# Optimization experiments

Hardware: AMD Instinct MI355X
Metric: run time of the kernel (lower is better)

The kernel has to match this reference:

```python
import jax, jax.numpy as jnp
import numpy as np

C, K, D_LLM = 32, 16, 768
B, L, D_MODEL = 8, 512, 256
H, D_KEYS = 8, 32
TEMP = 1.0 / np.sqrt(D_KEYS)


def setup_inputs() -> dict:
    key = jax.random.key(0)
    ks = jax.random.split(key, 8)
    topk = jax.random.normal(ks[0], (C, K, D_LLM), dtype=jnp.float32)
    ts_emb = jax.random.normal(ks[1], (B, L, D_MODEL), dtype=jnp.float32)
    probs = jax.random.uniform(ks[2], (B, L, C), dtype=jnp.float32)
    probs = probs / jnp.sum(probs, axis=-1, keepdims=True)  # soft cluster probabilities
    scale = 0.02  # keep pre-softmax logits in a stable range
    q_proj = jax.random.normal(ks[3], (C, H * D_KEYS, D_MODEL + 1), dtype=jnp.float32) * scale
    k_proj = jax.random.normal(ks[4], (C, H * D_KEYS, D_LLM + 1), dtype=jnp.float32) * scale
    v_proj = jax.random.normal(ks[5], (C, H * D_KEYS, D_LLM + 1), dtype=jnp.float32) * scale
    out_w = jax.random.normal(ks[6], (C, H, D_KEYS, D_LLM), dtype=jnp.float32) * scale
    out_b = jax.random.normal(ks[7], (C, D_LLM), dtype=jnp.float32) * scale
    return {"topk_token_embeddings": topk, "ts_emb": ts_emb, "cluster_probs": probs,
            "q_proj": q_proj, "k_proj": k_proj, "v_proj": v_proj,
            "out_w": out_w, "out_b": out_b}


def reference(topk_token_embeddings, ts_emb, cluster_probs, q_proj, k_proj, v_proj, out_w, out_b):
    b, l, _ = ts_emb.shape
    c, k, d_llm = topk_token_embeddings.shape
    # per-cluster Q/K/V projections (weights have an extra trailing bias column)
    q = jnp.einsum('bld,cgd->blcg', ts_emb, q_proj[..., :-1]) + q_proj[..., -1]
    q = q.reshape(b, l, c, H, D_KEYS)
    kk = jnp.einsum('ckd,cgd->kcg', topk_token_embeddings, k_proj[..., :-1]) + k_proj[..., -1]
    kk = kk.reshape(k, c, H, D_KEYS)
    v = jnp.einsum('ckd,cgd->kcg', topk_token_embeddings, v_proj[..., :-1]) + v_proj[..., -1]
    v = v.reshape(k, c, H, D_KEYS)
    # cross attention over the k retrieved tokens, per cluster and head
    att = jnp.einsum('blchd,kchd->bchlk', q, kk)  # (B,c,H,L,k)
    att = jax.nn.softmax(TEMP * att, axis=-1)  # dropout disabled (eval)
    out_v = jnp.einsum('bchlk,kchd->bclhd', att, v)
    aligned = jnp.einsum('bclhd,chde->blce', out_v, out_w) + out_b  # (B,L,c,d_llm)
    fused = jnp.sum(aligned * cluster_probs[:, :, :, None], axis=-2)  # (B,L,d_llm)
    return fused
```

## Files before the change

kernel.cpp:

```cpp
#include <hip/hip_runtime.h>
#include <hip/hip_bf16.h>

#define C_   32
#define K_   16
#define DLLM 768
#define DM   256
#define H_   8
#define DK   32
#define G_   256
#define BL   4096
#define NN   4096
#define E_   768
#define LDP  4160
#define TEMPF 0.17677669529663687f
#define SCL2  0.2550348647f

typedef __attribute__((ext_vector_type(8))) short bf16x8;
typedef __attribute__((ext_vector_type(4))) float f32x4;
typedef unsigned int u32;

__device__ __forceinline__ unsigned short f2bf(float f) {
    unsigned int u = __float_as_uint(f);
    unsigned int r = (u + 0x7fffu + ((u >> 16) & 1u)) >> 16;
    return (unsigned short)r;
}
__device__ __forceinline__ float bf2f(unsigned int u) {
    return __uint_as_float(u << 16);
}

__device__ __forceinline__ void gl16(const void* g, void* l) {
    __builtin_amdgcn_global_load_lds(
        (const __attribute__((address_space(1))) u32*)g,
        (__attribute__((address_space(3))) u32*)l, 16, 0, 0);
}

__global__ __launch_bounds__(256) void k1_kv(const float* __restrict__ topk,
                                             const float* __restrict__ kp,
                                             const float* __restrict__ vp,
                                             float* __restrict__ kk,
                                             float* __restrict__ vv) {
    const int cl  = blockIdx.x;
    const int nq  = blockIdx.y;
    const int mat = blockIdx.z;
    const float* src = mat ? vp : kp;
    float* dst       = mat ? vv : kk;

    const int t = threadIdx.x;
    const int lane = t & 63, w = t >> 6;
    const int c15 = lane & 15, gg = lane >> 4;

    __shared__ unsigned short a_lds[16 * 776];
#pragma unroll
    for (int i = 0; i < 12; ++i) {
        const int e = (i * 256 + t) * 4;
        const int r = e / 768, d = e - r * 768;
        float4 v4 = *reinterpret_cast<const float4*>(topk + (size_t)cl * 12288 + e);
        unsigned u0, u1;
        asm("v_cvt_pk_bf16_f32 %0, %1, %2" : "=v"(u0) : "v"(v4.x), "v"(v4.y));
        asm("v_cvt_pk_bf16_f32 %0, %1, %2" : "=v"(u1) : "v"(v4.z), "v"(v4.w));
        uint2 p; p.x = u0; p.y = u1;
        *reinterpret_cast<uint2*>(&a_lds[r * 776 + d]) = p;
    }
    __syncthreads();

    const int gcol = nq * 64 + w * 16 + c15;
    const float* bp = src + (size_t)(cl * G_ + gcol) * (DLLM + 1);
    const float bias = bp[DLLM];

    f32x4 acc = {};
    float4 b0 = *reinterpret_cast<const float4*>(bp + gg * 8);
    float4 b1 = *reinterpret_cast<const float4*>(bp + gg * 8 + 4);
#pragma unroll
    for (int s = 0; s < 24; ++s) {
        float4 n0, n1;
        if (s < 23) {
            n0 = *reinterpret_cast<const float4*>(bp + (s + 1) * 32 + gg * 8);
            n1 = *reinterpret_cast<const float4*>(bp + (s + 1) * 32 + gg * 8 + 4);
        }
        union { unsigned u[4]; bf16x8 v; } bb;
        asm("v_cvt_pk_bf16_f32 %0, %1, %2" : "=v"(bb.u[0]) : "v"(b0.x), "v"(b0.y));
        asm("v_cvt_pk_bf16_f32 %0, %1, %2" : "=v"(bb.u[1]) : "v"(b0.z), "v"(b0.w));
        asm("v_cvt_pk_bf16_f32 %0, %1, %2" : "=v"(bb.u[2]) : "v"(b1.x), "v"(b1.y));
        asm("v_cvt_pk_bf16_f32 %0, %1, %2" : "=v"(bb.u[3]) : "v"(b1.z), "v"(b1.w));
        bf16x8 af = *reinterpret_cast<const bf16x8*>(&a_lds[c15 * 776 + s * 32 + gg * 8]);
        acc = __builtin_amdgcn_mfma_f32_16x16x32_bf16(af, bb.v, acc, 0, 0, 0);
        b0 = n0; b1 = n1;
    }

#pragma unroll
    for (int i = 0; i < 4; ++i) {
        const int row = gg * 4 + i;
        dst[(size_t)(cl * K_ + row) * G_ + gcol] = acc[i] + bias;
    }
}

__global__ __launch_bounds__(256) void k0_cvt(const float* __restrict__ ts,
                                              const float* __restrict__ probs,
                                              const float* __restrict__ outb,
                                              unsigned short* __restrict__ tsb,
                                              unsigned short* __restrict__ P,
                                              unsigned short* __restrict__ VWt) {
    const int bid = blockIdx.x, t = threadIdx.x;
    if (bid < 1024) {
        const int idx = bid * 1024 + t * 4;
        float4 v = *reinterpret_cast<const float4*>(ts + idx);
        uint2 o;
        o.x = f2bf(v.x) | ((unsigned)f2bf(v.y) << 16);
        o.y = f2bf(v.z) | ((unsigned)f2bf(v.w) << 16);
        *reinterpret_cast<uint2*>(tsb + idx) = o;
    } else if (bid < 1056) {
        const int b2 = bid - 1024;
        const int row = b2 * 128 + (t >> 1);
        const int ch = (t & 1) * 16;
        unsigned short o[16];
#pragma unroll
        for (int j = 0; j < 16; ++j) o[j] = f2bf(probs[row * 32 + ch + j]);
        uint4 u0, u1;
        u0.x = o[0] | (o[1] << 16);  u0.y = o[2] | (o[3] << 16);
        u0.z = o[4] | (o[5] << 16);  u0.w = o[6] | (o[7] << 16);
        u1.x = o[8] | (o[9] << 16);  u1.y = o[10] | (o[11] << 16);
        u1.z = o[12] | (o[13] << 16); u1.w = o[14] | (o[15] << 16);
        unsigned short* dst = P + (size_t)row * LDP + 4096 + ch;
        *reinterpret_cast<uint4*>(dst) = u0;
        *reinterpret_cast<uint4*>(dst + 8) = u1;
        uint4 z = {0u, 0u, 0u, 0u};
        unsigned short* pz = P + (size_t)row * LDP + 4128 + ch;
        *reinterpret_cast<uint4*>(pz) = z;
        *reinterpret_cast<uint4*>(pz + 8) = z;
    } else {
        const int idx = (bid - 1056) * 256 + t;
        const int e = idx >> 5, cc = idx & 31;
        VWt[(size_t)e * LDP + 4096 + cc] = f2bf(outb[cc * E_ + e]);
        VWt[(size_t)e * LDP + 4128 + cc] = 0;
    }
}

__global__ __launch_bounds__(768) void k23(const float* __restrict__ qp,
                                           const float* __restrict__ kk,
                                           const float* __restrict__ ow,
                                           const float* __restrict__ vv,
                                           unsigned short* __restrict__ A2t,
                                           float* __restrict__ abias,
                                           unsigned short* __restrict__ VWt) {
    const int c = blockIdx.x, h = blockIdx.y;
    const int t = threadIdx.x;
    __shared__ float kk_l[K_][DK];
    __shared__ float v_l[K_][DK];
    __shared__ float bq_l[DK];
    if (t < 512) {
        int k = t / DK, d = t % DK;
        kk_l[k][d] = kk[(size_t)(c * K_ + k) * G_ + h * DK + d];
        v_l[k][d]  = vv[(size_t)(c * K_ + k) * G_ + h * DK + d];
    }
    if (t < DK)
        bq_l[t] = qp[(size_t)(c * G_ + h * DK + t) * (DM + 1) + DM];
    __syncthreads();
    const int ch = c * H_ + h;
    {
        const int e = t;
        float acc[K_];
#pragma unroll
        for (int k = 0; k < K_; ++k) acc[k] = 0.f;
        for (int d = 0; d < DK; ++d) {
            float w = ow[((size_t)ch * DK + d) * E_ + e];
#pragma unroll
            for (int k = 0; k < K_; ++k) acc[k] += w * v_l[k][d];
        }
#pragma unroll
        for (int k = 0; k < K_; ++k)
            VWt[(size_t)e * LDP + ch * 16 + k] = f2bf(acc[k]);
    }
    if (t < 256) {
        const int m = t;
        float acc[K_];
#pragma unroll
        for (int k = 0; k < K_; ++k) acc[k] = 0.f;
        for (int d = 0; d < DK; ++d) {
            float wq = qp[(size_t)(c * G_ + h * DK + d) * (DM + 1) + m];
#pragma unroll
            for (int k = 0; k < K_; ++k) acc[k] += wq * kk_l[k][d];
        }
#pragma unroll
        for (int k = 0; k < K_; ++k)
            A2t[(size_t)(ch * 16 + k) * DM + m] = f2bf(acc[k] * SCL2);
        if (m < K_) {
            float s = 0.f;
#pragma unroll
            for (int d = 0; d < DK; ++d) s += bq_l[d] * kk_l[m][d];
            abias[ch * 16 + m] = s * SCL2;
        }
    }
}

__global__ __launch_bounds__(256, 2) void k4_att(const unsigned short* __restrict__ A2t,
                                                 const unsigned short* __restrict__ tsb,
                                                 const float* __restrict__ abias,
                                                 const float* __restrict__ probs,
                                                 unsigned short* __restrict__ P) {
    const int n0  = blockIdx.x * 128;
    const int bl0 = blockIdx.y * 256;
    const int t = threadIdx.x;
    const int lane = t & 63, w = t >> 6;
    const int wr = w >> 1, wc = w & 1;
    const int c = lane & 15, g = lane >> 4;
    const int rsl = (c >> 1) & 3;

    __shared__ unsigned short a_l[3][128 * 32];
    __shared__ unsigned short b_l[3][256 * 32];
    __shared__ float ab_l[128];
    __shared__ float pb_l[256];

    if (t < 128) ab_l[t] = abias[n0 + t];
    pb_l[t] = probs[(size_t)(bl0 + t) * C_ + (n0 >> 7)];

    const int srow = t >> 2;
    const int sw = ((t & 3) ^ ((t >> 3) & 3)) * 8;

#define K4_STAGE(buf, kt)                                                         \
    {                                                                             \
        const int col_ = (kt) * 32 + sw;                                          \
        _Pragma("unroll")                                                         \
        for (int j = 0; j < 2; ++j)                                               \
            gl16(A2t + (size_t)(n0 + j * 64 + srow) * DM + col_,                  \
                 &a_l[buf][j * 2048 + t * 8]);                                    \
        _Pragma("unroll")                                                         \
        for (int j = 0; j < 4; ++j)                                               \
            gl16(tsb + (size_t)(bl0 + j * 64 + srow) * DM + col_,                 \
                 &b_l[buf][j * 2048 + t * 8]);                                    \
    }

    K4_STAGE(0, 0)
    K4_STAGE(1, 1)
    asm volatile("s_waitcnt lgkmcnt(0)" ::: "memory");

    f32x4 acc[4][8] = {};

#pragma unroll
    for (int kt = 0; kt < 8; ++kt) {
        const int bcur = kt % 3;
        if (kt < 6) {
            K4_STAGE((kt + 2) % 3, kt + 2)
            asm volatile("s_waitcnt vmcnt(12)" ::: "memory");
        } else if (kt == 6) {
            asm volatile("s_waitcnt vmcnt(6)" ::: "memory");
        } else {
            asm volatile("s_waitcnt vmcnt(0)" ::: "memory");
        }
        asm volatile("s_barrier" ::: "memory");
        bf16x8 af[4], bfr[8];
#pragma unroll
        for (int a = 0; a < 4; ++a)
            af[a] = *reinterpret_cast<const bf16x8*>(
                &a_l[bcur][(wr * 64 + a * 16 + c) * 32 + (g ^ rsl) * 8]);
#pragma unroll
        for (int b = 0; b < 8; ++b)
            bfr[b] = *reinterpret_cast<const bf16x8*>(
                &b_l[bcur][(wc * 128 + b * 16 + c) * 32 + (g ^ rsl) * 8]);
#pragma unroll
        for (int a = 0; a < 4; ++a)
#pragma unroll
            for (int b = 0; b < 8; ++b)
                acc[a][b] = __builtin_amdgcn_mfma_f32_16x16x32_bf16(af[a], bfr[b], acc[a][b], 0, 0, 0);
        if (kt < 7)
            asm volatile("s_barrier" ::: "memory");
    }
#undef K4_STAGE

#pragma unroll
    for (int a = 0; a < 4; ++a) {
        const int nbase = wr * 64 + a * 16 + g * 4;
#pragma unroll
        for (int b = 0; b < 8; ++b) {
            const int bll = wc * 128 + b * 16 + c;
            float e0 = __builtin_amdgcn_exp2f(acc[a][b][0] + ab_l[nbase + 0]);
            float e1 = __builtin_amdgcn_exp2f(acc[a][b][1] + ab_l[nbase + 1]);
            float e2 = __builtin_amdgcn_exp2f(acc[a][b][2] + ab_l[nbase + 2]);
            float e3 = __builtin_amdgcn_exp2f(acc[a][b][3] + ab_l[nbase + 3]);
            float s = (e0 + e1) + (e2 + e3);
            s += __shfl_xor(s, 16);
            s += __shfl_xor(s, 32);
            const float pv = pb_l[bll] * __builtin_amdgcn_rcpf(s);
            unsigned r0, r1;
            float p0 = e0 * pv, p1 = e1 * pv, p2 = e2 * pv, p3 = e3 * pv;
            asm("v_cvt_pk_bf16_f32 %0, %1, %2" : "=v"(r0) : "v"(p0), "v"(p1));
            asm("v_cvt_pk_bf16_f32 %0, %1, %2" : "=v"(r1) : "v"(p2), "v"(p3));
            uint2 o; o.x = r0; o.y = r1;
            *reinterpret_cast<uint2*>(P + (size_t)(bl0 + bll) * LDP + n0 + nbase) = o;
        }
    }
}

__global__ __launch_bounds__(256, 3) void k5_out(const unsigned short* __restrict__ P,
                                                 const unsigned short* __restrict__ VWt,
                                                 unsigned short* __restrict__ part) {
    const int wg = blockIdx.x;
    const int xcd = wg & 7;
    const int local = wg >> 3;
    const int bl0 = (xcd * 4 + (local & 3)) * 128;
    const int e0  = ((local >> 2) & 3) * 192;
    const int ks  = local >> 4;

    const int t = threadIdx.x;
    const int lane = t & 63, w = t >> 6;
    const int wr = w >> 1, wc = w & 1;
    const int c = lane & 15, g = lane >> 4;
    const int rsl = (c >> 1) & 3;

    __shared__ unsigned short a_l[2][128 * 32];
    __shared__ unsigned short b_l[2][192 * 32];

    const int nstart = ks * 704;
    const int nsteps = (ks == 5) ? 20 : 22;

    const int srow = t >> 2;
    const int sw = ((t & 3) ^ ((t >> 3) & 3)) * 8;

#define K5_STAGE(buf, kt)                                                         \
    {                                                                             \
        const int col_ = nstart + (kt) * 32 + sw;                                 \
        _Pragma("unroll")                                                         \
        for (int j = 0; j < 2; ++j)                                               \
            gl16(P + (size_t)(bl0 + j * 64 + srow) * LDP + col_,                  \
                 &a_l[buf][j * 2048 + t * 8]);                                    \
        _Pragma("unroll")                                                         \
        for (int j = 0; j < 3; ++j)                                               \
            gl16(VWt + (size_t)(e0 + j * 64 + srow) * LDP + col_,                 \
                 &b_l[buf][j * 2048 + t * 8]);                                    \
    }

    K5_STAGE(0, 0)

    f32x4 acc[4][6] = {};
    for (int kt = 0; kt < nsteps; ++kt) {
        const int bcur = kt & 1;
        if (kt + 1 < nsteps) {
            K5_STAGE(bcur ^ 1, kt + 1)
            asm volatile("s_waitcnt vmcnt(5)" ::: "memory");
        } else {
            asm volatile("s_waitcnt vmcnt(0)" ::: "memory");
        }
        asm volatile("s_barrier" ::: "memory");
        bf16x8 af[4], bfr[6];
#pragma unroll
        for (int a = 0; a < 4; ++a)
            af[a] = *reinterpret_cast<const bf16x8*>(
                &a_l[bcur][(wr * 64 + a * 16 + c) * 32 + (g ^ rsl) * 8]);
#pragma unroll
        for (int b = 0; b < 6; ++b)
            bfr[b] = *reinterpret_cast<const bf16x8*>(
                &b_l[bcur][(wc * 96 + b * 16 + c) * 32 + (g ^ rsl) * 8]);
#pragma unroll
        for (int a = 0; a < 4; ++a)
#pragma unroll
            for (int b = 0; b < 6; ++b)
                acc[a][b] = __builtin_amdgcn_mfma_f32_16x16x32_bf16(af[a], bfr[b], acc[a][b], 0, 0, 0);
        if (kt + 1 < nsteps)
            asm volatile("s_barrier" ::: "memory");
    }
#undef K5_STAGE

    unsigned short* pp = part + ((size_t)ks * BL + bl0) * E_ + e0;
#pragma unroll
    for (int a = 0; a < 4; ++a)
#pragma unroll
        for (int b = 0; b < 6; ++b)
#pragma unroll
            for (int i = 0; i < 4; ++i)
                pp[(size_t)(wr * 64 + a * 16 + g * 4 + i) * E_ + wc * 96 + b * 16 + c] =
                    f2bf(acc[a][b][i]);
}

__global__ __launch_bounds__(256) void k6_red(const unsigned short* __restrict__ part,
                                              float* __restrict__ out) {
    const size_t base = ((size_t)blockIdx.x * 256 + threadIdx.x) * 8;
    float s[8] = {};
#pragma unroll
    for (int ks = 0; ks < 6; ++ks) {
        uint4 v = *reinterpret_cast<const uint4*>(part + (size_t)ks * (BL * E_) + base);
        const unsigned u[4] = {v.x, v.y, v.z, v.w};
#pragma unroll
        for (int j = 0; j < 4; ++j) {
            s[2 * j]     += bf2f(u[j] & 0xffffu);
            s[2 * j + 1] += bf2f(u[j] >> 16);
        }
    }
    *reinterpret_cast<float4*>(out + base)     = make_float4(s[0], s[1], s[2], s[3]);
    *reinterpret_cast<float4*>(out + base + 4) = make_float4(s[4], s[5], s[6], s[7]);
}

extern "C" void kernel_launch(void* const* d_in, const int* in_sizes, int n_in,
                              void* d_out, int out_size, void* d_ws, size_t ws_size,
                              hipStream_t stream) {
    const float* topk  = (const float*)d_in[0];
    const float* ts    = (const float*)d_in[1];
    const float* probs = (const float*)d_in[2];
    const float* qp    = (const float*)d_in[3];
    const float* kp    = (const float*)d_in[4];
    const float* vp    = (const float*)d_in[5];
    const float* ow    = (const float*)d_in[6];
    const float* ob    = (const float*)d_in[7];
    float* out = (float*)d_out;

    char* wp = (char*)d_ws;
    float* kk            = (float*)wp;           wp += 524288;
    float* vv            = (float*)wp;           wp += 524288;
    float* ab            = (float*)wp;           wp += 16384;
    unsigned short* tsb  = (unsigned short*)wp;  wp += 2097152;
    unsigned short* A2t  = (unsigned short*)wp;  wp += 2097152;
    unsigned short* VWt  = (unsigned short*)wp;  wp += (size_t)E_ * LDP * 2;
    unsigned short* P    = (unsigned short*)wp;  wp += (size_t)BL * LDP * 2;
    unsigned short* part = (unsigned short*)wp;

    k1_kv <<<dim3(32, 4, 2), 256, 0, stream>>>(topk, kp, vp, kk, vv);
    k0_cvt<<<1152,           256, 0, stream>>>(ts, probs, ob, tsb, P, VWt);
    k23   <<<dim3(32, 8),    768, 0, stream>>>(qp, kk, ow, vv, A2t, ab, VWt);
    k4_att<<<dim3(32, 16),   256, 0, stream>>>(A2t, tsb, ab, probs, P);
    k5_out<<<768,            256, 0, stream>>>(P, VWt, part);
    k6_red<<<1536,           256, 0, stream>>>(part, out);
}
```

Baseline: 99.21 us.

## Merge prep kernels, transpose probs, shrink attention tile for occupancy

Folds the K/V projection kernel and the conversion kernel into one launch, which removes a launch and its serialization gap. It adds a block range that transposes cluster_probs so the attention kernel loads per-cluster probabilities with coalesced reads. The attention-logit kernel moves from a 128x256 tile with triple buffering to a 128x128 tile with double buffering. That halves the accumulators and LDS, allowing 4 blocks per CU, and doubles the grid. The trade-off is less reuse of the A2t tile per block and a shallower prefetch pipeline.

```diff
diff --git a/kernel.cpp b/kernel.cpp
--- a/kernel.cpp
+++ b/kernel.cpp
@@ -34,82 +34,81 @@
         (__attribute__((address_space(3))) u32*)l, 16, 0, 0);
 }
 
-__global__ __launch_bounds__(256) void k1_kv(const float* __restrict__ topk,
-                                             const float* __restrict__ kp,
-                                             const float* __restrict__ vp,
-                                             float* __restrict__ kk,
-                                             float* __restrict__ vv) {
-    const int cl  = blockIdx.x;
-    const int nq  = blockIdx.y;
-    const int mat = blockIdx.z;
-    const float* src = mat ? vp : kp;
-    float* dst       = mat ? vv : kk;
-
-    const int t = threadIdx.x;
-    const int lane = t & 63, w = t >> 6;
-    const int c15 = lane & 15, gg = lane >> 4;
-
+__global__ __launch_bounds__(256) void k01(const float* __restrict__ topk,
+                                           const float* __restrict__ kp,
+                                           const float* __restrict__ vp,
+                                           float* __restrict__ kk,
+                                           float* __restrict__ vv,
+                                           const float* __restrict__ ts,
+                                           const float* __restrict__ probs,
+                                           const float* __restrict__ outb,
+                                           unsigned short* __restrict__ tsb,
+                                           unsigned short* __restrict__ P,
+                                           unsigned short* __restrict__ VWt,
+                                           float* __restrict__ probsT) {
+    const int bid = blockIdx.x, t = threadIdx.x;
     __shared__ unsigned short a_lds[16 * 776];
-#pragma unroll
-    for (int i = 0; i < 12; ++i) {
-        const int e = (i * 256 + t) * 4;
-        const int r = e / 768, d = e - r * 768;
-        float4 v4 = *reinterpret_cast<const float4*>(topk + (size_t)cl * 12288 + e);
-        unsigned u0, u1;
-        asm("v_cvt_pk_bf16_f32 %0, %1, %2" : "=v"(u0) : "v"(v4.x), "v"(v4.y));
-        asm("v_cvt_pk_bf16_f32 %0, %1, %2" : "=v"(u1) : "v"(v4.z), "v"(v4.w));
-        uint2 p; p.x = u0; p.y = u1;
-        *reinterpret_cast<uint2*>(&a_lds[r * 776 + d]) = p;
-    }
-    __syncthreads();
-
-    const int gcol = nq * 64 + w * 16 + c15;
-    const float* bp = src + (size_t)(cl * G_ + gcol) * (DLLM + 1);
-    const float bias = bp[DLLM];
-
-    f32x4 acc = {};
-    float4 b0 = *reinterpret_cast<const float4*>(bp + gg * 8);
-    float4 b1 = *reinterpret_cast<const float4*>(bp + gg * 8 + 4);
-#pragma unroll
-    for (int s = 0; s < 24; ++s) {
-        float4 n0, n1;
-        if (s < 23) {
-            n0 = *reinterpret_cast<const float4*>(bp + (s + 1) * 32 + gg * 8);
-            n1 = *reinterpret_cast<const float4*>(bp + (s + 1) * 32 + gg * 8 + 4);
-        }
-        union { unsigned u[4]; bf16x8 v; } bb;
-        asm("v_cvt_pk_bf16_f32 %0, %1, %2" : "=v"(bb.u[0]) : "v"(b0.x), "v"(b0.y));
-        asm("v_cvt_pk_bf16_f32 %0, %1, %2" : "=v"(bb.u[1]) : "v"(b0.z), "v"(b0.w));
-        asm("v_cvt_pk_bf16_f32 %0, %1, %2" : "=v"(bb.u[2]) : "v"(b1.x), "v"(b1.y));
-        asm("v_cvt_pk_bf16_f32 %0, %1, %2" : "=v"(bb.u[3]) : "v"(b1.z), "v"(b1.w));
-        bf16x8 af = *reinterpret_cast<const bf16x8*>(&a_lds[c15 * 776 + s * 32 + gg * 8]);
-        acc = __builtin_amdgcn_mfma_f32_16x16x32_bf16(af, bb.v, acc, 0, 0, 0);
-        b0 = n0; b1 = n1;
-    }
-
-#pragma unroll
-    for (int i = 0; i < 4; ++i) {
-        const int row = gg * 4 + i;
-        dst[(size_t)(cl * K_ + row) * G_ + gcol] = acc[i] + bias;
-    }
-}
-
-__global__ __launch_bounds__(256) void k0_cvt(const float* __restrict__ ts,
-                                              const float* __restrict__ probs,
-                                              const float* __restrict__ outb,
-                                              unsigned short* __restrict__ tsb,
-                                              unsigned short* __restrict__ P,
-                                              unsigned short* __restrict__ VWt) {
-    const int bid = blockIdx.x, t = threadIdx.x;
-    if (bid < 1024) {
-        const int idx = bid * 1024 + t * 4;
+
+    if (bid < 256) {
+        const int cl  = bid & 31;
+        const int nq  = (bid >> 5) & 3;
+        const int mat = bid >> 7;
+        const float* src = mat ? vp : kp;
+        float* dst       = mat ? vv : kk;
+
+        const int lane = t & 63, w = t >> 6;
+        const int c15 = lane & 15, gg = lane >> 4;
+
+#pragma unroll
+        for (int i = 0; i < 12; ++i) {
+            const int e = (i * 256 + t) * 4;
+            const int r = e / 768, d = e - r * 768;
+            float4 v4 = *reinterpret_cast<const float4*>(topk + (size_t)cl * 12288 + e);
+            unsigned u0, u1;
+            asm("v_cvt_pk_bf16_f32 %0, %1, %2" : "=v"(u0) : "v"(v4.x), "v"(v4.y));
+            asm("v_cvt_pk_bf16_f32 %0, %1, %2" : "=v"(u1) : "v"(v4.z), "v"(v4.w));
+            uint2 p; p.x = u0; p.y = u1;
+            *reinterpret_cast<uint2*>(&a_lds[r * 776 + d]) = p;
+        }
+        __syncthreads();
+
+        const int gcol = nq * 64 + w * 16 + c15;
+        const float* bp = src + (size_t)(cl * G_ + gcol) * (DLLM + 1);
+        const float bias = bp[DLLM];
+
+        f32x4 acc = {};
+        float4 b0 = *reinterpret_cast<const float4*>(bp + gg * 8);
+        float4 b1 = *reinterpret_cast<const float4*>(bp + gg * 8 + 4);
+#pragma unroll
+        for (int s = 0; s < 24; ++s) {
+            float4 n0, n1;
+            if (s < 23) {
+                n0 = *reinterpret_cast<const float4*>(bp + (s + 1) * 32 + gg * 8);
+                n1 = *reinterpret_cast<const float4*>(bp + (s + 1) * 32 + gg * 8 + 4);
+            }
+            union { unsigned u[4]; bf16x8 v; } bb;
+            asm("v_cvt_pk_bf16_f32 %0, %1, %2" : "=v"(bb.u[0]) : "v"(b0.x), "v"(b0.y));
+            asm("v_cvt_pk_bf16_f32 %0, %1, %2" : "=v"(bb.u[1]) : "v"(b0.z), "v"(b0.w));
+            asm("v_cvt_pk_bf16_f32 %0, %1, %2" : "=v"(bb.u[2]) : "v"(b1.x), "v"(b1.y));
+            asm("v_cvt_pk_bf16_f32 %0, %1, %2" : "=v"(bb.u[3]) : "v"(b1.z), "v"(b1.w));
+            bf16x8 af = *reinterpret_cast<const bf16x8*>(&a_lds[c15 * 776 + s * 32 + gg * 8]);
+            acc = __builtin_amdgcn_mfma_f32_16x16x32_bf16(af, bb.v, acc, 0, 0, 0);
+            b0 = n0; b1 = n1;
+        }
+#pragma unroll
+        for (int i = 0; i < 4; ++i) {
+            const int row = gg * 4 + i;
+            dst[(size_t)(cl * K_ + row) * G_ + gcol] = acc[i] + bias;
+        }
+    } else if (bid < 1280) {
+        const int idx = (bid - 256) * 1024 + t * 4;
         float4 v = *reinterpret_cast<const float4*>(ts + idx);
         uint2 o;
         o.x = f2bf(v.x) | ((unsigned)f2bf(v.y) << 16);
         o.y = f2bf(v.z) | ((unsigned)f2bf(v.w) << 16);
         *reinterpret_cast<uint2*>(tsb + idx) = o;
-    } else if (bid < 1056) {
-        const int b2 = bid - 1024;
+    } else if (bid < 1312) {
+        const int b2 = bid - 1280;
         const int row = b2 * 128 + (t >> 1);
         const int ch = (t & 1) * 16;
         unsigned short o[16];
@@ -127,11 +126,27 @@
         unsigned short* pz = P + (size_t)row * LDP + 4128 + ch;
         *reinterpret_cast<uint4*>(pz) = z;
         *reinterpret_cast<uint4*>(pz + 8) = z;
-    } else {
-        const int idx = (bid - 1056) * 256 + t;
+    } else if (bid < 1408) {
+        const int idx = (bid - 1312) * 256 + t;
         const int e = idx >> 5, cc = idx & 31;
         VWt[(size_t)e * LDP + 4096 + cc] = f2bf(outb[cc * E_ + e]);
         VWt[(size_t)e * LDP + 4128 + cc] = 0;
+    } else {
+        float* tl = reinterpret_cast<float*>(a_lds);
+        const int bl0p = (bid - 1408) * 128;
+#pragma unroll
+        for (int i = 0; i < 16; ++i) {
+            const int row = i * 8 + (t >> 5);
+            const int cc = t & 31;
+            tl[row * 33 + cc] = probs[(size_t)(bl0p + row) * C_ + cc];
+        }
+        __syncthreads();
+#pragma unroll
+        for (int j = 0; j < 16; ++j) {
+            const int cc = j * 2 + (t >> 7);
+            const int bl = t & 127;
+            probsT[(size_t)cc * BL + bl0p + bl] = tl[bl * 33 + cc];
+        }
     }
 }
 
@@ -192,26 +207,26 @@
     }
 }
 
-__global__ __launch_bounds__(256, 2) void k4_att(const unsigned short* __restrict__ A2t,
+__global__ __launch_bounds__(256, 4) void k4_att(const unsigned short* __restrict__ A2t,
                                                  const unsigned short* __restrict__ tsb,
                                                  const float* __restrict__ abias,
-                                                 const float* __restrict__ probs,
+                                                 const float* __restrict__ probsT,
                                                  unsigned short* __restrict__ P) {
     const int n0  = blockIdx.x * 128;
-    const int bl0 = blockIdx.y * 256;
+    const int bl0 = blockIdx.y * 128;
     const int t = threadIdx.x;
     const int lane = t & 63, w = t >> 6;
     const int wr = w >> 1, wc = w & 1;
     const int c = lane & 15, g = lane >> 4;
     const int rsl = (c >> 1) & 3;
 
-    __shared__ unsigned short a_l[3][128 * 32];
-    __shared__ unsigned short b_l[3][256 * 32];
+    __shared__ unsigned short a_l[2][128 * 32];
+    __shared__ unsigned short b_l[2][128 * 32];
     __shared__ float ab_l[128];
-    __shared__ float pb_l[256];
+    __shared__ float pb_l[128];
 
     if (t < 128) ab_l[t] = abias[n0 + t];
-    pb_l[t] = probs[(size_t)(bl0 + t) * C_ + (n0 >> 7)];
+    else         pb_l[t - 128] = probsT[(size_t)(n0 >> 7) * BL + bl0 + (t - 128)];
 
     const int srow = t >> 2;
     const int sw = ((t & 3) ^ ((t >> 3) & 3)) * 8;
@@ -224,42 +239,39 @@
             gl16(A2t + (size_t)(n0 + j * 64 + srow) * DM + col_,                  \
                  &a_l[buf][j * 2048 + t * 8]);                                    \
         _Pragma("unroll")                                                         \
-        for (int j = 0; j < 4; ++j)                                               \
+        for (int j = 0; j < 2; ++j)                                               \
             gl16(tsb + (size_t)(bl0 + j * 64 + srow) * DM + col_,                 \
                  &b_l[buf][j * 2048 + t * 8]);                                    \
     }
 
     K4_STAGE(0, 0)
-    K4_STAGE(1, 1)
     asm volatile("s_waitcnt lgkmcnt(0)" ::: "memory");
 
-    f32x4 acc[4][8] = {};
+    f32x4 acc[4][4] = {};
 
 #pragma unroll
     for (int kt = 0; kt < 8; ++kt) {
-        const int bcur = kt % 3;
-        if (kt < 6) {
-            K4_STAGE((kt + 2) % 3, kt + 2)
-            asm volatile("s_waitcnt vmcnt(12)" ::: "memory");
-        } else if (kt == 6) {
-            asm volatile("s_waitcnt vmcnt(6)" ::: "memory");
+        const int bcur = kt & 1;
+        if (kt < 7) {
+            K4_STAGE(bcur ^ 1, kt + 1)
+            asm volatile("s_waitcnt vmcnt(4)" ::: "memory");
         } else {
             asm volatile("s_waitcnt vmcnt(0)" ::: "memory");
         }
         asm volatile("s_barrier" ::: "memory");
-        bf16x8 af[4], bfr[8];
+        bf16x8 af[4], bfr[4];
 #pragma unroll
         for (int a = 0; a < 4; ++a)
             af[a] = *reinterpret_cast<const bf16x8*>(
                 &a_l[bcur][(wr * 64 + a * 16 + c) * 32 + (g ^ rsl) * 8]);
 #pragma unroll
-        for (int b = 0; b < 8; ++b)
+        for (int b = 0; b < 4; ++b)
             bfr[b] = *reinterpret_cast<const bf16x8*>(
-                &b_l[bcur][(wc * 128 + b * 16 + c) * 32 + (g ^ rsl) * 8]);
+                &b_l[bcur][(wc * 64 + b * 16 + c) * 32 + (g ^ rsl) * 8]);
 #pragma unroll
         for (int a = 0; a < 4; ++a)
 #pragma unroll
-            for (int b = 0; b < 8; ++b)
+            for (int b = 0; b < 4; ++b)
                 acc[a][b] = __builtin_amdgcn_mfma_f32_16x16x32_bf16(af[a], bfr[b], acc[a][b], 0, 0, 0);
         if (kt < 7)
             asm volatile("s_barrier" ::: "memory");
@@ -270,8 +282,8 @@
     for (int a = 0; a < 4; ++a) {
         const int nbase = wr * 64 + a * 16 + g * 4;
 #pragma unroll
-        for (int b = 0; b < 8; ++b) {
-            const int bll = wc * 128 + b * 16 + c;
+        for (int b = 0; b < 4; ++b) {
+            const int bll = wc * 64 + b * 16 + c;
             float e0 = __builtin_amdgcn_exp2f(acc[a][b][0] + ab_l[nbase + 0]);
             float e1 = __builtin_amdgcn_exp2f(acc[a][b][1] + ab_l[nbase + 1]);
             float e2 = __builtin_amdgcn_exp2f(acc[a][b][2] + ab_l[nbase + 2]);
@@ -405,16 +417,17 @@
     float* kk            = (float*)wp;           wp += 524288;
     float* vv            = (float*)wp;           wp += 524288;
     float* ab            = (float*)wp;           wp += 16384;
+    float* probsT        = (float*)wp;           wp += 524288;
     unsigned short* tsb  = (unsigned short*)wp;  wp += 2097152;
     unsigned short* A2t  = (unsigned short*)wp;  wp += 2097152;
     unsigned short* VWt  = (unsigned short*)wp;  wp += (size_t)E_ * LDP * 2;
     unsigned short* P    = (unsigned short*)wp;  wp += (size_t)BL * LDP * 2;
     unsigned short* part = (unsigned short*)wp;
 
-    k1_kv <<<dim3(32, 4, 2), 256, 0, stream>>>(topk, kp, vp, kk, vv);
-    k0_cvt<<<1152,           256, 0, stream>>>(ts, probs, ob, tsb, P, VWt);
-    k23   <<<dim3(32, 8),    768, 0, stream>>>(qp, kk, ow, vv, A2t, ab, VWt);
-    k4_att<<<dim3(32, 16),   256, 0, stream>>>(A2t, tsb, ab, probs, P);
-    k5_out<<<768,            256, 0, stream>>>(P, VWt, part);
-    k6_red<<<1536,           256, 0, stream>>>(part, out);
-}
+    k01   <<<1440,         256, 0, stream>>>(topk, kp, vp, kk, vv,
+                                             ts, probs, ob, tsb, P, VWt, probsT);
+    k23   <<<dim3(32, 8),  768, 0, stream>>>(qp, kk, ow, vv, A2t, ab, VWt);
+    k4_att<<<dim3(32, 32), 256, 0, stream>>>(A2t, tsb, ab, probsT, P);
+    k5_out<<<768,          256, 0, stream>>>(P, VWt, part);
+    k6_red<<<1536,         256, 0, stream>>>(part, out);
+}
```

Result: faster. 95.11 us, median of 2 (-4.1%).
